# Performance work log

Measured on AMD Instinct MI355X. Metric: run time of the kernel, lower is better.

## Reference

```python
import jax, jax.numpy as jnp
import numpy as np


def setup_inputs() -> dict:
    key = jax.random.key(0)
    k1, k2 = jax.random.split(key)
    qs = jax.random.normal(k1, (64, 32, 128), dtype=jnp.float32)   # (n_queries, n_query_tokens, dim)
    ps = jax.random.normal(k2, (64, 1024, 128), dtype=jnp.float32)  # (n_docs, n_doc_tokens, dim)
    return {"qs": qs, "ps": ps}


def reference(qs, ps):
    # ColBERT MaxSim: for each (query b, doc c), sum over query tokens of the
    # max similarity against all doc tokens.
    # scores[b,c,n,s] = sum_d qs[b,n,d] * ps[c,s,d]
    sim = jnp.einsum('bnd,csd->bcns', qs, ps)  # (n_q, n_d, tok_q, tok_d)
    scores = sim.max(axis=3).sum(axis=2)       # (n_q, n_d)
    return scores
```

## Files before the change

kernel.cpp:

```cpp
#include <hip/hip_runtime.h>
#include <stdint.h>


typedef __bf16 bf16x8 __attribute__((ext_vector_type(8)));
typedef float floatx16 __attribute__((ext_vector_type(16)));

#define QS_N (64u * 32u * 128u)
#define PS_N (64u * 1024u * 128u)

__device__ ushort g_bf[QS_N + PS_N];

__global__ __launch_bounds__(256) void cvt_kernel(const float* __restrict__ qs,
                                                  const float* __restrict__ ps) {
  const int nq4 = QS_N / 4;
  const int n4 = (QS_N + PS_N) / 4;
  int i = blockIdx.x * 256 + threadIdx.x;
  if (i >= n4) return;
  float4 f;
  if (i < nq4) {
    f = ((const float4*)qs)[i];
  } else {
    f = ((const float4*)ps)[i - nq4];
  }
  union { ushort4 s; struct { __bf16 a, b, c, d; } h; } o;
  o.h.a = (__bf16)f.x; o.h.b = (__bf16)f.y; o.h.c = (__bf16)f.z; o.h.d = (__bf16)f.w;
  ((ushort4*)g_bf)[i] = o.s;
}

union FragU { uint4 u; bf16x8 v; };

__device__ inline bf16x8 load_frag_bf16(const ushort* p) {
  FragU f;
  f.u = *(const uint4*)p;
  return f.v;
}

__device__ inline float rmax16(const floatx16& a) {
  float m0 = fmaxf(fmaxf(a[0], a[1]), fmaxf(a[2], a[3]));
  float m1 = fmaxf(fmaxf(a[4], a[5]), fmaxf(a[6], a[7]));
  float m2 = fmaxf(fmaxf(a[8], a[9]), fmaxf(a[10], a[11]));
  float m3 = fmaxf(fmaxf(a[12], a[13]), fmaxf(a[14], a[15]));
  return fmaxf(fmaxf(m0, m1), fmaxf(m2, m3));
}

#define ZERO16 {0, 0, 0, 0, 0, 0, 0, 0, 0, 0, 0, 0, 0, 0, 0, 0}

#define TILE_COMPUTE(ABUF)                                                     \
  {                                                                            \
    floatx16 acc0 = ZERO16, acc1 = ZERO16;                                     \
    _Pragma("unroll") for (int k = 0; k < 8; ++k) {                            \
      acc0 = __builtin_amdgcn_mfma_f32_32x32x16_bf16(ABUF[k], qf[0][k], acc0, 0, 0, 0); \
      acc1 = __builtin_amdgcn_mfma_f32_32x32x16_bf16(ABUF[k], qf[1][k], acc1, 0, 0, 0); \
    }                                                                          \
    vmax[0] = fmaxf(vmax[0], rmax16(acc0));                                    \
    vmax[1] = fmaxf(vmax[1], rmax16(acc1));                                    \
    floatx16 acc2 = ZERO16, acc3 = ZERO16;                                     \
    _Pragma("unroll") for (int k = 0; k < 8; ++k) {                            \
      acc2 = __builtin_amdgcn_mfma_f32_32x32x16_bf16(ABUF[k], qf[2][k], acc2, 0, 0, 0); \
      acc3 = __builtin_amdgcn_mfma_f32_32x32x16_bf16(ABUF[k], qf[3][k], acc3, 0, 0, 0); \
    }                                                                          \
    vmax[2] = fmaxf(vmax[2], rmax16(acc2));                                    \
    vmax[3] = fmaxf(vmax[3], rmax16(acc3));                                    \
  }

__global__ __launch_bounds__(256, 2) void maxsim_kernel(float* __restrict__ out) {
  const ushort* qsb = g_bf;
  const ushort* psb = g_bf + QS_N;

  const int lane = threadIdx.x & 63;
  const int wave = threadIdx.x >> 6;

  const int xcd = blockIdx.x & 7;
  const int slot = blockIdx.x >> 3;
  const int c = xcd * 8 + (slot >> 4);
  const int bg = slot & 15;
  const int b0 = bg * 4;
  const int row = lane & 31;
  const int koff = (lane >> 5) * 8;

  __shared__ ushort lds_q[4 * 8 * 64 * 8];
  {
    uint4* dst = (uint4*)lds_q;
#pragma unroll
    for (int i = 0; i < 8; ++i) {
      const int id = threadIdx.x + i * 256;
      const int l = id & 63;
      const int k = (id >> 6) & 7;
      const int b = id >> 9;
      const int goff = ((b0 + b) * 32 + (l & 31)) * 128 + k * 16 + (l >> 5) * 8;
      dst[id] = *(const uint4*)(qsb + goff);
    }
  }
  __syncthreads();

  const ushort* lq = lds_q + lane * 8;
  bf16x8 qf[4][8];
#pragma unroll
  for (int b = 0; b < 4; ++b)
#pragma unroll
    for (int k = 0; k < 8; ++k)
      qf[b][k] = *(const bf16x8*)(lq + (b * 8 + k) * 512);

  const int pbase = (c * 1024 + wave * 256 + row) * 128 + koff;

  bf16x8 a0[8], a1[8];
#pragma unroll
  for (int k = 0; k < 8; ++k) a0[k] = load_frag_bf16(psb + pbase + k * 16);

  float vmax[4];
#pragma unroll
  for (int b = 0; b < 4; ++b) vmax[b] = -3.4e38f;

#pragma unroll 1
  for (int t = 0; t < 8; t += 2) {
#pragma unroll
    for (int k = 0; k < 8; ++k)
      a1[k] = load_frag_bf16(psb + pbase + (t + 1) * 4096 + k * 16);
    TILE_COMPUTE(a0)
    int t2 = t + 2;
    if (t2 > 7) t2 = 0;
#pragma unroll
    for (int k = 0; k < 8; ++k)
      a0[k] = load_frag_bf16(psb + pbase + t2 * 4096 + k * 16);
    TILE_COMPUTE(a1)
  }

#pragma unroll
  for (int b = 0; b < 4; ++b) vmax[b] = fmaxf(vmax[b], __shfl_xor(vmax[b], 32, 64));

  __shared__ float red[4][4][32];
  if (lane < 32) {
#pragma unroll
    for (int b = 0; b < 4; ++b) red[wave][b][lane] = vmax[b];
  }
  __syncthreads();
  if (threadIdx.x < 128) {
    const int b = threadIdx.x >> 5;
    const int n = threadIdx.x & 31;
    float m = fmaxf(fmaxf(red[0][b][n], red[1][b][n]), fmaxf(red[2][b][n], red[3][b][n]));
#pragma unroll
    for (int o = 16; o > 0; o >>= 1) m += __shfl_xor(m, o, 32);
    if (n == 0) out[(b0 + b) * 64 + c] = m;
  }
}

extern "C" void kernel_launch(void* const* d_in, const int* in_sizes, int n_in,
                              void* d_out, int out_size, void* d_ws, size_t ws_size,
                              hipStream_t stream) {
  const float* qs = (const float*)d_in[0];
  const float* ps = (const float*)d_in[1];
  float* out = (float*)d_out;
  (void)d_ws; (void)ws_size;

  const int n4 = (int)((QS_N + PS_N) / 4);
  cvt_kernel<<<(n4 + 255) / 256, 256, 0, stream>>>(qs, ps);
  maxsim_kernel<<<dim3(64 * 16), dim3(256), 0, stream>>>(out);
}
```

Before: 116.7 us.

## Share doc tiles via LDS with async global-to-LDS double buffering

Each block now covers one doc and 8 queries, with each wave holding 2 queries in registers. All four waves stream the same 32-token doc tile through a double-buffered LDS buffer, filled by global_load_lds direct copies. This replaces the old scheme where each wave loaded its own doc slice from global into registers, so each doc fragment is fetched once per block and reused by all waves. In exchange there is a block-wide barrier every tile, LDS reads inside the MFMA loop, and half as many blocks (512), which lowers parallelism.

Measured after the change: 111.5 us. -4.5%, faster.

```diff
diff --git a/kernel.cpp b/kernel.cpp
--- a/kernel.cpp
+++ b/kernel.cpp
@@ -16,23 +16,10 @@
   const int n4 = (QS_N + PS_N) / 4;
   int i = blockIdx.x * 256 + threadIdx.x;
   if (i >= n4) return;
-  float4 f;
-  if (i < nq4) {
-    f = ((const float4*)qs)[i];
-  } else {
-    f = ((const float4*)ps)[i - nq4];
-  }
+  float4 f = (i < nq4) ? ((const float4*)qs)[i] : ((const float4*)ps)[i - nq4];
   union { ushort4 s; struct { __bf16 a, b, c, d; } h; } o;
   o.h.a = (__bf16)f.x; o.h.b = (__bf16)f.y; o.h.c = (__bf16)f.z; o.h.d = (__bf16)f.w;
   ((ushort4*)g_bf)[i] = o.s;
-}
-
-union FragU { uint4 u; bf16x8 v; };
-
-__device__ inline bf16x8 load_frag_bf16(const ushort* p) {
-  FragU f;
-  f.u = *(const uint4*)p;
-  return f.v;
 }
 
 __device__ inline float rmax16(const floatx16& a) {
@@ -43,27 +30,15 @@
   return fmaxf(fmaxf(m0, m1), fmaxf(m2, m3));
 }
 
+typedef __attribute__((address_space(1))) const void gas_t;
+typedef __attribute__((address_space(3))) void las_t;
+__device__ inline void gload_lds16(const ushort* g, ushort* l) {
+  __builtin_amdgcn_global_load_lds((gas_t*)g, (las_t*)l, 16, 0, 0);
+}
+
 #define ZERO16 {0, 0, 0, 0, 0, 0, 0, 0, 0, 0, 0, 0, 0, 0, 0, 0}
 
-#define TILE_COMPUTE(ABUF)                                                     \
-  {                                                                            \
-    floatx16 acc0 = ZERO16, acc1 = ZERO16;                                     \
-    _Pragma("unroll") for (int k = 0; k < 8; ++k) {                            \
-      acc0 = __builtin_amdgcn_mfma_f32_32x32x16_bf16(ABUF[k], qf[0][k], acc0, 0, 0, 0); \
-      acc1 = __builtin_amdgcn_mfma_f32_32x32x16_bf16(ABUF[k], qf[1][k], acc1, 0, 0, 0); \
-    }                                                                          \
-    vmax[0] = fmaxf(vmax[0], rmax16(acc0));                                    \
-    vmax[1] = fmaxf(vmax[1], rmax16(acc1));                                    \
-    floatx16 acc2 = ZERO16, acc3 = ZERO16;                                     \
-    _Pragma("unroll") for (int k = 0; k < 8; ++k) {                            \
-      acc2 = __builtin_amdgcn_mfma_f32_32x32x16_bf16(ABUF[k], qf[2][k], acc2, 0, 0, 0); \
-      acc3 = __builtin_amdgcn_mfma_f32_32x32x16_bf16(ABUF[k], qf[3][k], acc3, 0, 0, 0); \
-    }                                                                          \
-    vmax[2] = fmaxf(vmax[2], rmax16(acc2));                                    \
-    vmax[3] = fmaxf(vmax[3], rmax16(acc3));                                    \
-  }
-
-__global__ __launch_bounds__(256, 2) void maxsim_kernel(float* __restrict__ out) {
+__global__ __launch_bounds__(256) void maxsim_kernel(float* __restrict__ out) {
   const ushort* qsb = g_bf;
   const ushort* psb = g_bf + QS_N;
 
@@ -72,75 +47,70 @@
 
   const int xcd = blockIdx.x & 7;
   const int slot = blockIdx.x >> 3;
-  const int c = xcd * 8 + (slot >> 4);
-  const int bg = slot & 15;
-  const int b0 = bg * 4;
+  const int c = xcd * 8 + (slot >> 3);
+  const int bg = slot & 7;
+  const int qb0 = bg * 8 + wave * 2;
+
   const int row = lane & 31;
-  const int koff = (lane >> 5) * 8;
+  const int hi8 = (lane >> 5) * 8;
 
-  __shared__ ushort lds_q[4 * 8 * 64 * 8];
-  {
-    uint4* dst = (uint4*)lds_q;
+  bf16x8 qf[2][8];
 #pragma unroll
-    for (int i = 0; i < 8; ++i) {
-      const int id = threadIdx.x + i * 256;
-      const int l = id & 63;
-      const int k = (id >> 6) & 7;
-      const int b = id >> 9;
-      const int goff = ((b0 + b) * 32 + (l & 31)) * 128 + k * 16 + (l >> 5) * 8;
-      dst[id] = *(const uint4*)(qsb + goff);
-    }
+  for (int bb = 0; bb < 2; ++bb) {
+    const ushort* q = qsb + ((qb0 + bb) * 32 + row) * 128 + hi8;
+#pragma unroll
+    for (int k = 0; k < 8; ++k)
+      qf[bb][k] = *(const bf16x8*)(q + k * 16);
+  }
+
+  __shared__ __align__(16) ushort lds_p[2][4096];
+
+  const int pg_lane = (c * 1024 + row) * 128 + hi8;
+
+#pragma unroll
+  for (int jj = 0; jj < 2; ++jj) {
+    const int j = wave * 2 + jj;
+    gload_lds16(psb + pg_lane + j * 16, &lds_p[0][j * 512]);
   }
   __syncthreads();
 
-  const ushort* lq = lds_q + lane * 8;
-  bf16x8 qf[4][8];
-#pragma unroll
-  for (int b = 0; b < 4; ++b)
-#pragma unroll
-    for (int k = 0; k < 8; ++k)
-      qf[b][k] = *(const bf16x8*)(lq + (b * 8 + k) * 512);
-
-  const int pbase = (c * 1024 + wave * 256 + row) * 128 + koff;
-
-  bf16x8 a0[8], a1[8];
-#pragma unroll
-  for (int k = 0; k < 8; ++k) a0[k] = load_frag_bf16(psb + pbase + k * 16);
-
-  float vmax[4];
-#pragma unroll
-  for (int b = 0; b < 4; ++b) vmax[b] = -3.4e38f;
+  float vmax0 = -3.4e38f, vmax1 = -3.4e38f;
+  int cb = 0;
 
 #pragma unroll 1
-  for (int t = 0; t < 8; t += 2) {
+  for (int t = 0; t < 32; ++t) {
+    if (t < 31) {
+      const int soff = (t + 1) * 32 * 128;
 #pragma unroll
-    for (int k = 0; k < 8; ++k)
-      a1[k] = load_frag_bf16(psb + pbase + (t + 1) * 4096 + k * 16);
-    TILE_COMPUTE(a0)
-    int t2 = t + 2;
-    if (t2 > 7) t2 = 0;
+      for (int jj = 0; jj < 2; ++jj) {
+        const int j = wave * 2 + jj;
+        gload_lds16(psb + pg_lane + soff + j * 16, &lds_p[cb ^ 1][j * 512]);
+      }
+    }
+    const ushort* lp = &lds_p[cb][0] + lane * 8;
+    floatx16 acc0 = ZERO16, acc1 = ZERO16;
 #pragma unroll
-    for (int k = 0; k < 8; ++k)
-      a0[k] = load_frag_bf16(psb + pbase + t2 * 4096 + k * 16);
-    TILE_COMPUTE(a1)
+    for (int k = 0; k < 8; ++k) {
+      bf16x8 af = *(const bf16x8*)(lp + k * 512);
+      acc0 = __builtin_amdgcn_mfma_f32_32x32x16_bf16(af, qf[0][k], acc0, 0, 0, 0);
+      acc1 = __builtin_amdgcn_mfma_f32_32x32x16_bf16(af, qf[1][k], acc1, 0, 0, 0);
+    }
+    vmax0 = fmaxf(vmax0, rmax16(acc0));
+    vmax1 = fmaxf(vmax1, rmax16(acc1));
+    __syncthreads();
+    cb ^= 1;
   }
 
+  vmax0 = fmaxf(vmax0, __shfl_xor(vmax0, 32, 64));
+  vmax1 = fmaxf(vmax1, __shfl_xor(vmax1, 32, 64));
 #pragma unroll
-  for (int b = 0; b < 4; ++b) vmax[b] = fmaxf(vmax[b], __shfl_xor(vmax[b], 32, 64));
-
-  __shared__ float red[4][4][32];
-  if (lane < 32) {
-#pragma unroll
-    for (int b = 0; b < 4; ++b) red[wave][b][lane] = vmax[b];
+  for (int o = 16; o > 0; o >>= 1) {
+    vmax0 += __shfl_xor(vmax0, o, 64);
+    vmax1 += __shfl_xor(vmax1, o, 64);
   }
-  __syncthreads();
-  if (threadIdx.x < 128) {
-    const int b = threadIdx.x >> 5;
-    const int n = threadIdx.x & 31;
-    float m = fmaxf(fmaxf(red[0][b][n], red[1][b][n]), fmaxf(red[2][b][n], red[3][b][n]));
-#pragma unroll
-    for (int o = 16; o > 0; o >>= 1) m += __shfl_xor(m, o, 32);
-    if (n == 0) out[(b0 + b) * 64 + c] = m;
+  if (lane == 0) {
+    out[(qb0 + 0) * 64 + c] = vmax0;
+    out[(qb0 + 1) * 64 + c] = vmax1;
   }
 }
 
@@ -154,5 +124,5 @@
 
   const int n4 = (int)((QS_N + PS_N) / 4);
   cvt_kernel<<<(n4 + 255) / 256, 256, 0, stream>>>(qs, ps);
-  maxsim_kernel<<<dim3(64 * 16), dim3(256), 0, stream>>>(out);
+  maxsim_kernel<<<dim3(512), dim3(256), 0, stream>>>(out);
 }
```
